# Kernel tuning notes

Measured on AMD Instinct MI355X. Metric: run time of the kernel, lower is better.

Reference implementation:

```python
import jax, jax.numpy as jnp
import numpy as np

DIM = 384
EPS = 1e-12  # F.normalize default eps


def setup_inputs() -> dict:
    key = jax.random.key(0)
    ks = jax.random.split(key, 6)
    b, c, h, w = 4, DIM, 64, 64
    x = jax.random.normal(ks[0], (b, c, h, w), dtype=jnp.float32)
    gamma = jnp.ones((c,), dtype=jnp.float32)  # WanRMS_norm gamma, init ones
    # 1x1 convs are per-pixel linear maps: [out_c, in_c] weight + bias
    w_qkv = jax.random.normal(ks[1], (3 * c, c), dtype=jnp.float32) * (1.0 / np.sqrt(c))
    b_qkv = jax.random.normal(ks[2], (3 * c,), dtype=jnp.float32) * 0.01
    w_proj = jax.random.normal(ks[3], (c, c), dtype=jnp.float32) * (1.0 / np.sqrt(c))
    b_proj = jax.random.normal(ks[4], (c,), dtype=jnp.float32) * 0.01
    return {"x": x, "gamma": gamma, "w_qkv": w_qkv, "b_qkv": b_qkv,
            "w_proj": w_proj, "b_proj": b_proj}


def reference(x, gamma, w_qkv, b_qkv, w_proj, b_proj):
    b, c, h, w = x.shape
    identity = x
    # WanRMS_norm: F.normalize over channel dim * sqrt(dim) * gamma
    l2 = jnp.sqrt(jnp.sum(x * x, axis=1, keepdims=True))
    xn = x / jnp.maximum(l2, EPS) * jnp.sqrt(jnp.float32(c)) * gamma[None, :, None, None]
    # 1x1 conv qkv: [b, 3c, h, w]
    qkv = jnp.einsum("bchw,oc->bohw", xn, w_qkv) + b_qkv[None, :, None, None]
    # flatten spatial -> tokens: [b, 3c, s] -> q/k/v each [b, s, c]
    s = h * w
    qkv = qkv.reshape(b, 3 * c, s).transpose(0, 2, 1)  # [b, s, 3c]
    q, k, v = jnp.split(qkv, 3, axis=-1)
    # single-head scaled dot-product attention (non-causal, as in Wan SDPA call)
    scores = jnp.einsum("bqc,bkc->bqk", q, k) / jnp.sqrt(jnp.float32(c))
    attn = jax.nn.softmax(scores, axis=-1)
    out = jnp.einsum("bqk,bkc->bqc", attn, v)  # [b, s, c]
    out = out.transpose(0, 2, 1).reshape(b, c, h, w)
    # 1x1 proj conv + residual
    out = jnp.einsum("bchw,oc->bohw", out, w_proj) + b_proj[None, :, None, None]
    return out + identity
```

## Files before the change

### kernel.cpp

```cpp
#include <hip/hip_runtime.h>
#include <cstdint>
#include <cstddef>

typedef __bf16 bf16;
typedef __bf16 bf16x8 __attribute__((ext_vector_type(8)));
typedef float  f32x4 __attribute__((ext_vector_type(4)));
typedef float  f32x16 __attribute__((ext_vector_type(16)));
typedef int    i32x4 __attribute__((ext_vector_type(4)));
typedef int    i32x8 __attribute__((ext_vector_type(8)));

#define MFMA16(a, b, c) __builtin_amdgcn_mfma_f32_16x16x32_bf16((a), (b), (c), 0, 0, 0)
#define MFMA_MX(a, b, c) \
    __builtin_amdgcn_mfma_scale_f32_32x32x64_f8f6f4((a), (b), (c), 0, 0, 0, 0x7F, 0, 0x7F)

__device__ __forceinline__ uint8_t to_fp8(float v) {
    return (uint8_t)(__builtin_amdgcn_cvt_pk_fp8_f32(v, v, 0, false) & 0xff);
}

__device__ __forceinline__ i32x8 ld32(const void* p) {
    i32x4 a = *(const i32x4*)p;
    i32x4 b = *(const i32x4*)((const char*)p + 16);
    i32x8 r;
    r[0] = a[0]; r[1] = a[1]; r[2] = a[2]; r[3] = a[3];
    r[4] = b[0]; r[5] = b[1]; r[6] = b[2]; r[7] = b[3];
    return r;
}

__device__ __forceinline__ void gload16(const void* g, void* l) {
    __builtin_amdgcn_global_load_lds(
        (const __attribute__((address_space(1))) unsigned int*)g,
        (__attribute__((address_space(3))) unsigned int*)l,
        16, 0, 0);
}

__global__ __launch_bounds__(256) void convert_w(
    const float* __restrict__ wqkv, const float* __restrict__ wproj,
    bf16* __restrict__ wq, bf16* __restrict__ wp)
{
    int t = blockIdx.x * 256 + threadIdx.x;
    if (t < 1152 * 384) wq[t] = (bf16)wqkv[t];
    else                wp[t - 1152 * 384] = (bf16)wproj[t - 1152 * 384];
}

__global__ __launch_bounds__(64) void norm_kernel(
    const float* __restrict__ x, const float* __restrict__ gamma,
    bf16* __restrict__ xn)
{
    __shared__ float sG[384];
    int tid = threadIdx.x;
    for (int i = tid; i < 384; i += 64) sG[i] = gamma[i];
    __syncthreads();
    int t = blockIdx.x * 64 + tid;
    int b = t >> 12, p = t & 4095;
    const float* xb = x + (size_t)(b * 384) * 4096 + p;
    float ss = 0.f;
    for (int c = 0; c < 384; ++c) { float v = xb[(size_t)c * 4096]; ss += v * v; }
    float scale = 19.595917942265423f / fmaxf(sqrtf(ss), 1e-12f);
    bf16* o = xn + (size_t)t * 384;
    for (int c0 = 0; c0 < 384; c0 += 8) {
        bf16x8 v8;
#pragma unroll
        for (int j = 0; j < 8; ++j)
            v8[j] = (bf16)(xb[(size_t)(c0 + j) * 4096] * scale * sG[c0 + j]);
        *(bf16x8*)(o + c0) = v8;
    }
}

__global__ __launch_bounds__(256) void gemm_bt(
    const bf16* __restrict__ A, const bf16* __restrict__ B,
    const float* __restrict__ bias_m, const float* __restrict__ bias_n,
    const float* __restrict__ resid, void* __restrict__ Cout,
    int mode, int ldc)
{
    __shared__ bf16 sA[128 * 72];
    __shared__ bf16 sB[128 * 72];
    const int tid = threadIdx.x;
    const int l = tid & 63, w = tid >> 6;
    const int lo = l & 15, hi = l >> 4;
    const int wm = w >> 1, wn = w & 1;
    const int m0 = blockIdx.y * 128, n0 = blockIdx.x * 128;

    f32x4 acc[4][4] = {};

    for (int kt = 0; kt < 6; ++kt) {
        __syncthreads();
        const int k0 = kt * 64;
#pragma unroll
        for (int i = 0; i < 5; ++i) {
            int ci = i * 256 + tid;
            if (ci < 1152) {
                int row = ci / 9, off = ci % 9;
                gload16(A + (size_t)(m0 + row) * 384 + k0 + off * 8, (char*)sA + ci * 16);
                gload16(B + (size_t)(n0 + row) * 384 + k0 + off * 8, (char*)sB + ci * 16);
            }
        }
        __syncthreads();
#pragma unroll
        for (int ks = 0; ks < 2; ++ks) {
            bf16x8 af[4], bfr[4];
#pragma unroll
            for (int t = 0; t < 4; ++t)
                af[t] = *(const bf16x8*)(sA + (wm * 64 + t * 16 + lo) * 72 + ks * 32 + hi * 8);
#pragma unroll
            for (int t = 0; t < 4; ++t)
                bfr[t] = *(const bf16x8*)(sB + (wn * 64 + t * 16 + lo) * 72 + ks * 32 + hi * 8);
#pragma unroll
            for (int rt = 0; rt < 4; ++rt)
#pragma unroll
                for (int ct = 0; ct < 4; ++ct)
                    acc[rt][ct] = MFMA16(af[rt], bfr[ct], acc[rt][ct]);
        }
    }

#pragma unroll
    for (int rt = 0; rt < 4; ++rt) {
#pragma unroll
        for (int ct = 0; ct < 4; ++ct) {
            int mb = m0 + wm * 64 + rt * 16 + hi * 4;
            int n  = n0 + wn * 64 + ct * 16 + lo;
            if (mode == 0) {
                uint8_t* C = (uint8_t*)Cout;
                float bn = bias_n[n];
#pragma unroll
                for (int r = 0; r < 4; ++r)
                    C[(size_t)(mb + r) * ldc + n] = to_fp8(acc[rt][ct][r] + bn);
            } else if (mode == 1) {
                uint8_t* C = (uint8_t*)Cout;
#pragma unroll
                for (int r = 0; r < 4; ++r)
                    C[(size_t)(mb + r) * ldc + n] = to_fp8(acc[rt][ct][r] + bias_m[mb + r]);
            } else {
                float* O = (float*)Cout;
                int bb = n >> 12, p = n & 4095;
#pragma unroll
                for (int r = 0; r < 4; ++r) {
                    int m = mb + r;
                    size_t idx = ((size_t)(bb * 384 + m)) * 4096 + p;
                    O[idx] = acc[rt][ct][r] + bias_m[m] + resid[idx];
                }
            }
        }
    }
}

__device__ __forceinline__ void stage_tiles64(
    const uint8_t* __restrict__ qk, const uint8_t* __restrict__ vt,
    int kv0, uint8_t* sK, uint8_t* sV, int tid)
{
    const uint8_t* kb = qk + (size_t)kv0 * 768 + 384;
#pragma unroll
    for (int i = 0; i < 7; ++i) {
        int ci = i * 256 + tid;
        if (ci < 1600) {
            int row = ci / 25, off = ci % 25;
            gload16(kb + (size_t)row * 768 + off * 16, sK + ci * 16);
        }
    }
    const uint8_t* vb = vt + kv0;
#pragma unroll
    for (int i = 0; i < 8; ++i) {
        int ci = i * 256 + tid;
        if (ci < 1920) {
            int row = ci / 5, off = ci % 5;
            gload16(vb + (size_t)row * 16384 + off * 16, sV + ci * 16);
        }
    }
}

__global__ __launch_bounds__(256, 2) void flash_kernel(
    const uint8_t* __restrict__ qk, const uint8_t* __restrict__ vt,
    bf16* __restrict__ op0, bf16* __restrict__ op1, float* __restrict__ ml)
{
    __shared__ char smem[56320];
    uint8_t* sK = (uint8_t*)smem;
    uint8_t* sV = (uint8_t*)smem + 25600;
    const int tid = threadIdx.x;
    const int l = tid & 63, w = tid >> 6;
    const int l31 = l & 31, hi2 = l >> 5;
    const int wq = w >> 1, wd = w & 1;
    const int qt = blockIdx.x, bh = blockIdx.y;
    const int b = bh >> 1, half = bh & 1;
    const int q0 = b * 4096 + qt * 64;
    const int kvbase = b * 4096 + half * 2048;
    const float SC = 0.07362217057594547f;

    i32x8 qf[6];
    {
        const uint8_t* qrow = qk + (size_t)(q0 + wq * 32 + l31) * 768 + hi2 * 32;
#pragma unroll
        for (int ksw = 0; ksw < 6; ++ksw)
            qf[ksw] = ld32(qrow + ksw * 64);
    }

    f32x16 o[6] = {};
    float m = -1e30f, lsum = 0.f;

    for (int kt = 0; kt < 32; ++kt) {
        stage_tiles64(qk, vt, kvbase + kt * 64, sK, sV, tid);
        __syncthreads();

        f32x16 s0 = {}, s1 = {};
#pragma unroll
        for (int ksw = 0; ksw < 6; ++ksw) {
            i32x8 ak0 = ld32(sK + (size_t)l31 * 400 + ksw * 64 + hi2 * 32);
            i32x8 ak1 = ld32(sK + (size_t)(32 + l31) * 400 + ksw * 64 + hi2 * 32);
            s0 = MFMA_MX(ak0, qf[ksw], s0);
            s1 = MFMA_MX(ak1, qf[ksw], s1);
        }

        float mx = s0[0];
#pragma unroll
        for (int r = 1; r < 16; ++r) mx = fmaxf(mx, s0[r]);
#pragma unroll
        for (int r = 0; r < 16; ++r) mx = fmaxf(mx, s1[r]);
        mx = fmaxf(mx, __shfl_xor(mx, 32));
        if (__any(mx > m)) {
            float mn = fmaxf(m, mx);
            float alpha = exp2f((m - mn) * SC);
            m = mn;
            lsum *= alpha;
#pragma unroll
            for (int dt = 0; dt < 6; ++dt)
#pragma unroll
                for (int r = 0; r < 16; ++r) o[dt][r] *= alpha;
        }
        float p0[16], p1[16];
        float rs = 0.f;
        float msc = m * SC;
#pragma unroll
        for (int r = 0; r < 16; ++r) { p0[r] = exp2f(fmaf(s0[r], SC, -msc)); rs += p0[r]; }
#pragma unroll
        for (int r = 0; r < 16; ++r) { p1[r] = exp2f(fmaf(s1[r], SC, -msc)); rs += p1[r]; }
        rs += __shfl_xor(rs, 32);
        lsum += rs;

        int pk0[4], pk1[4];
#pragma unroll
        for (int i = 0; i < 4; ++i) {
            int d = __builtin_amdgcn_cvt_pk_fp8_f32(p0[4 * i], p0[4 * i + 1], 0, false);
            pk0[i] = __builtin_amdgcn_cvt_pk_fp8_f32(p0[4 * i + 2], p0[4 * i + 3], d, true);
            d = __builtin_amdgcn_cvt_pk_fp8_f32(p1[4 * i], p1[4 * i + 1], 0, false);
            pk1[i] = __builtin_amdgcn_cvt_pk_fp8_f32(p1[4 * i + 2], p1[4 * i + 3], d, true);
        }
        i32x8 pf;
#pragma unroll
        for (int i = 0; i < 4; ++i) {
            int x0 = __shfl_xor(pk0[i], 32);
            int x1 = __shfl_xor(pk1[i], 32);
            int own = hi2 ? pk1[i] : pk0[i];
            int oth = hi2 ? x1 : x0;
            pf[2 * i]     = hi2 ? oth : own;
            pf[2 * i + 1] = hi2 ? own : oth;
        }

#pragma unroll
        for (int dt = 0; dt < 6; ++dt) {
            i32x8 av = ld32(sV + (size_t)(wd * 192 + dt * 32 + l31) * 80 + hi2 * 32);
            o[dt] = MFMA_MX(av, pf, o[dt]);
        }

        __syncthreads();
    }

    float* tr = (float*)(smem + w * 4608);
    bf16* dst = half ? op1 : op0;
#pragma unroll
    for (int dt = 0; dt < 6; ++dt) {
#pragma unroll
        for (int r = 0; r < 16; ++r) {
            int d32 = (r & 3) + 8 * (r >> 2) + 4 * hi2;
            tr[l31 * 36 + d32] = o[dt][r];
        }
        f32x4 v0 = *(f32x4*)(tr + l31 * 36 + hi2 * 16 + 0);
        f32x4 v1 = *(f32x4*)(tr + l31 * 36 + hi2 * 16 + 4);
        f32x4 v2 = *(f32x4*)(tr + l31 * 36 + hi2 * 16 + 8);
        f32x4 v3 = *(f32x4*)(tr + l31 * 36 + hi2 * 16 + 12);
        bf16x8 h0, h1;
#pragma unroll
        for (int j = 0; j < 4; ++j) {
            h0[j] = (bf16)v0[j]; h0[4 + j] = (bf16)v1[j];
            h1[j] = (bf16)v2[j]; h1[4 + j] = (bf16)v3[j];
        }
        size_t tok = (size_t)(q0 + wq * 32 + l31);
        bf16* drow = dst + tok * 384 + wd * 192 + dt * 32 + hi2 * 16;
        *(bf16x8*)(drow + 0) = h0;
        *(bf16x8*)(drow + 8) = h1;
        __syncthreads();
    }
    if (wd == 0 && hi2 == 0) {
        int tok = q0 + wq * 32 + l31;
        ml[(size_t)(half * 16384 + tok) * 2 + 0] = m * SC;
        ml[(size_t)(half * 16384 + tok) * 2 + 1] = lsum;
    }
}

__global__ __launch_bounds__(256) void merge_kernel(
    const bf16* __restrict__ p0, const bf16* __restrict__ p1,
    const float* __restrict__ ml, bf16* __restrict__ ob)
{
    int tok = blockIdx.x * 4 + (threadIdx.x >> 6);
    int l = threadIdx.x & 63;
    float m0 = ml[(size_t)tok * 2 + 0], l0 = ml[(size_t)tok * 2 + 1];
    float m1 = ml[(size_t)(16384 + tok) * 2 + 0], l1 = ml[(size_t)(16384 + tok) * 2 + 1];
    float mM = fmaxf(m0, m1);
    float a0 = exp2f(m0 - mM), a1 = exp2f(m1 - mM);
    float inv = 1.0f / (a0 * l0 + a1 * l1);
    float w0 = a0 * inv, w1 = a1 * inv;
    if (l < 48) {
        size_t off = (size_t)tok * 384 + l * 8;
        bf16x8 v0 = *(const bf16x8*)(p0 + off);
        bf16x8 v1 = *(const bf16x8*)(p1 + off);
        bf16x8 r;
#pragma unroll
        for (int j = 0; j < 8; ++j)
            r[j] = (bf16)((float)v0[j] * w0 + (float)v1[j] * w1);
        *(bf16x8*)(ob + off) = r;
    }
}

extern "C" void kernel_launch(void* const* d_in, const int* in_sizes, int n_in,
                              void* d_out, int out_size, void* d_ws, size_t ws_size,
                              hipStream_t stream) {
    const float* x      = (const float*)d_in[0];
    const float* gamma  = (const float*)d_in[1];
    const float* w_qkv  = (const float*)d_in[2];
    const float* b_qkv  = (const float*)d_in[3];
    const float* w_proj = (const float*)d_in[4];
    const float* b_proj = (const float*)d_in[5];
    float* out = (float*)d_out;

    char* ws = (char*)d_ws;
    bf16* xn  = (bf16*)ws;    ws += (size_t)16384 * 384 * 2;
    uint8_t* qkb = (uint8_t*)ws; ws += (size_t)16384 * 768;
    uint8_t* vtb = (uint8_t*)ws; ws += (size_t)384 * 16384;
    bf16* ob  = (bf16*)ws;    ws += (size_t)16384 * 384 * 2;
    bf16* wq  = (bf16*)ws;    ws += (size_t)1152 * 384 * 2;
    bf16* wp  = (bf16*)ws;    ws += (size_t)384 * 384 * 2;
    float* mlb = (float*)ws;  ws += (size_t)2 * 16384 * 2 * 4;

    convert_w<<<2304, 256, 0, stream>>>(w_qkv, w_proj, wq, wp);
    norm_kernel<<<256, 64, 0, stream>>>(x, gamma, xn);
    gemm_bt<<<dim3(6, 128), 256, 0, stream>>>(xn, wq, nullptr, b_qkv, nullptr, qkb, 0, 768);
    gemm_bt<<<dim3(128, 3), 256, 0, stream>>>(wq + (size_t)768 * 384, xn,
                                              b_qkv + 768, nullptr, nullptr, vtb, 1, 16384);
    flash_kernel<<<dim3(64, 8), 256, 0, stream>>>(qkb, vtb, xn, ob, mlb);
    merge_kernel<<<4096, 256, 0, stream>>>(xn, ob, mlb, ob);
    gemm_bt<<<dim3(128, 3), 256, 0, stream>>>(wp, ob, b_proj, nullptr, x, out, 2, 0);
}
```

Baseline: 287.4 us.

## Fuse weight conversion, norm, QKV GEMMs, merge; add lazy rescale and priorities

Folds the weight-conversion kernel into the norm kernel, which now splits the channel reduction across four waves for more parallelism. It merges the QK and V GEMMs into one launch, and fuses the split-KV merge into the projection GEMM's B-tile load. In the flash kernel it adds a lazy max-rescale threshold, raised wave priority around the MFMA sections, tree max reductions, split row-sum accumulators and a linearized grid. The aim is fewer launches, less intermediate traffic and more latency hiding. The risks are the fp8/exp2 overflow margin of the threshold and recomputing merge weights per tile row.

```diff
diff --git a/kernel.cpp b/kernel.cpp
--- a/kernel.cpp
+++ b/kernel.cpp
@@ -33,44 +33,142 @@
         16, 0, 0);
 }
 
-__global__ __launch_bounds__(256) void convert_w(
+__global__ __launch_bounds__(256) void norm_kernel(
+    const float* __restrict__ x, const float* __restrict__ gamma,
     const float* __restrict__ wqkv, const float* __restrict__ wproj,
-    bf16* __restrict__ wq, bf16* __restrict__ wp)
-{
-    int t = blockIdx.x * 256 + threadIdx.x;
-    if (t < 1152 * 384) wq[t] = (bf16)wqkv[t];
-    else                wp[t - 1152 * 384] = (bf16)wproj[t - 1152 * 384];
-}
-
-__global__ __launch_bounds__(64) void norm_kernel(
-    const float* __restrict__ x, const float* __restrict__ gamma,
-    bf16* __restrict__ xn)
-{
+    bf16* __restrict__ xn, bf16* __restrict__ wq, bf16* __restrict__ wp)
+{
+    const int tid = threadIdx.x;
+    const int blk = blockIdx.x;
+    if (blk >= 256) {
+        int t0 = (blk - 256) * 256 + tid;
+        for (int t = t0; t < 1152 * 384 + 384 * 384; t += 128 * 256) {
+            if (t < 1152 * 384) wq[t] = (bf16)wqkv[t];
+            else                wp[t - 1152 * 384] = (bf16)wproj[t - 1152 * 384];
+        }
+        return;
+    }
     __shared__ float sG[384];
-    int tid = threadIdx.x;
-    for (int i = tid; i < 384; i += 64) sG[i] = gamma[i];
+    __shared__ float sS[4][64];
+    __shared__ float sScale[64];
+    const int w = tid >> 6, l = tid & 63;
+    for (int i = tid; i < 384; i += 256) sG[i] = gamma[i];
+    const int b = blk >> 6, p0 = (blk & 63) << 6;
+    const float* xb = x + ((size_t)b * 384) * 4096 + p0 + l;
+    const float* xc = xb + (size_t)(96 * w) * 4096;
+    float s0 = 0.f, s1 = 0.f;
+#pragma unroll 8
+    for (int c = 0; c < 96; c += 2) {
+        float v0 = xc[(size_t)c * 4096];
+        float v1 = xc[(size_t)(c + 1) * 4096];
+        s0 += v0 * v0; s1 += v1 * v1;
+    }
+    sS[w][l] = s0 + s1;
     __syncthreads();
-    int t = blockIdx.x * 64 + tid;
-    int b = t >> 12, p = t & 4095;
-    const float* xb = x + (size_t)(b * 384) * 4096 + p;
-    float ss = 0.f;
-    for (int c = 0; c < 384; ++c) { float v = xb[(size_t)c * 4096]; ss += v * v; }
-    float scale = 19.595917942265423f / fmaxf(sqrtf(ss), 1e-12f);
-    bf16* o = xn + (size_t)t * 384;
-    for (int c0 = 0; c0 < 384; c0 += 8) {
+    if (w == 0) {
+        float t = (sS[0][l] + sS[1][l]) + (sS[2][l] + sS[3][l]);
+        sScale[l] = 19.595917942265423f / fmaxf(sqrtf(t), 1e-12f);
+    }
+    __syncthreads();
+    float sc = sScale[l];
+    int tok = (b << 12) + p0 + l;
+    bf16* o = xn + (size_t)tok * 384 + 96 * w;
+    for (int c0 = 0; c0 < 96; c0 += 8) {
         bf16x8 v8;
 #pragma unroll
         for (int j = 0; j < 8; ++j)
-            v8[j] = (bf16)(xb[(size_t)(c0 + j) * 4096] * scale * sG[c0 + j]);
+            v8[j] = (bf16)(xc[(size_t)(c0 + j) * 4096] * sc * sG[96 * w + c0 + j]);
         *(bf16x8*)(o + c0) = v8;
     }
 }
 
-__global__ __launch_bounds__(256) void gemm_bt(
+__device__ __forceinline__ void gemm_core_bt(
+    bf16* sA, bf16* sB,
     const bf16* __restrict__ A, const bf16* __restrict__ B,
     const float* __restrict__ bias_m, const float* __restrict__ bias_n,
-    const float* __restrict__ resid, void* __restrict__ Cout,
-    int mode, int ldc)
+    uint8_t* __restrict__ Cout, const int mode, const int ldc,
+    const int m0, const int n0)
+{
+    const int tid = threadIdx.x;
+    const int l = tid & 63, w = tid >> 6;
+    const int lo = l & 15, hi = l >> 4;
+    const int wm = w >> 1, wn = w & 1;
+
+    f32x4 acc[4][4] = {};
+
+    for (int kt = 0; kt < 6; ++kt) {
+        __syncthreads();
+        const int k0 = kt * 64;
+#pragma unroll
+        for (int i = 0; i < 5; ++i) {
+            int ci = i * 256 + tid;
+            if (ci < 1152) {
+                int row = ci / 9, off = ci % 9;
+                gload16(A + (size_t)(m0 + row) * 384 + k0 + off * 8, (char*)sA + ci * 16);
+                gload16(B + (size_t)(n0 + row) * 384 + k0 + off * 8, (char*)sB + ci * 16);
+            }
+        }
+        __syncthreads();
+#pragma unroll
+        for (int ks = 0; ks < 2; ++ks) {
+            bf16x8 af[4], bfr[4];
+#pragma unroll
+            for (int t = 0; t < 4; ++t)
+                af[t] = *(const bf16x8*)(sA + (wm * 64 + t * 16 + lo) * 72 + ks * 32 + hi * 8);
+#pragma unroll
+            for (int t = 0; t < 4; ++t)
+                bfr[t] = *(const bf16x8*)(sB + (wn * 64 + t * 16 + lo) * 72 + ks * 32 + hi * 8);
+#pragma unroll
+            for (int rt = 0; rt < 4; ++rt)
+#pragma unroll
+                for (int ct = 0; ct < 4; ++ct)
+                    acc[rt][ct] = MFMA16(af[rt], bfr[ct], acc[rt][ct]);
+        }
+    }
+
+#pragma unroll
+    for (int rt = 0; rt < 4; ++rt) {
+#pragma unroll
+        for (int ct = 0; ct < 4; ++ct) {
+            int mb = m0 + wm * 64 + rt * 16 + hi * 4;
+            int n  = n0 + wn * 64 + ct * 16 + lo;
+            if (mode == 0) {
+                float bn = bias_n[n];
+#pragma unroll
+                for (int r = 0; r < 4; ++r)
+                    Cout[(size_t)(mb + r) * ldc + n] = to_fp8(acc[rt][ct][r] + bn);
+            } else {
+#pragma unroll
+                for (int r = 0; r < 4; ++r)
+                    Cout[(size_t)(mb + r) * ldc + n] = to_fp8(acc[rt][ct][r] + bias_m[mb + r]);
+            }
+        }
+    }
+}
+
+__global__ __launch_bounds__(256) void gemm_qkv(
+    const bf16* __restrict__ xn, const bf16* __restrict__ wq,
+    const float* __restrict__ b_qkv, uint8_t* __restrict__ qkb,
+    uint8_t* __restrict__ vtb)
+{
+    __shared__ bf16 sA[128 * 72];
+    __shared__ bf16 sB[128 * 72];
+    const int id = blockIdx.x;
+    if (id < 768) {
+        gemm_core_bt(sA, sB, xn, wq, nullptr, b_qkv, qkb, 0, 768,
+                     (id / 6) * 128, (id % 6) * 128);
+    } else {
+        const int t = id - 768;
+        gemm_core_bt(sA, sB, wq + (size_t)768 * 384, xn, b_qkv + 768, nullptr,
+                     vtb, 1, 16384, (t >> 7) * 128, (t & 127) * 128);
+    }
+}
+
+__global__ __launch_bounds__(256) void gemm_proj(
+    const bf16* __restrict__ wp, const bf16* __restrict__ p0,
+    const bf16* __restrict__ p1, const float* __restrict__ ml,
+    const float* __restrict__ b_proj, const float* __restrict__ x,
+    float* __restrict__ out)
 {
     __shared__ bf16 sA[128 * 72];
     __shared__ bf16 sB[128 * 72];
@@ -90,8 +188,22 @@
             int ci = i * 256 + tid;
             if (ci < 1152) {
                 int row = ci / 9, off = ci % 9;
-                gload16(A + (size_t)(m0 + row) * 384 + k0 + off * 8, (char*)sA + ci * 16);
-                gload16(B + (size_t)(n0 + row) * 384 + k0 + off * 8, (char*)sB + ci * 16);
+                gload16(wp + (size_t)(m0 + row) * 384 + k0 + off * 8, (char*)sA + ci * 16);
+                int tok = n0 + row;
+                float2 ml0 = *(const float2*)(ml + (size_t)tok * 2);
+                float2 ml1 = *(const float2*)(ml + (size_t)(16384 + tok) * 2);
+                float mM = fmaxf(ml0.x, ml1.x);
+                float a0 = exp2f(ml0.x - mM), a1 = exp2f(ml1.x - mM);
+                float inv = 1.0f / (a0 * ml0.y + a1 * ml1.y);
+                float w0 = a0 * inv, w1 = a1 * inv;
+                size_t boff = (size_t)tok * 384 + k0 + off * 8;
+                bf16x8 v0 = *(const bf16x8*)(p0 + boff);
+                bf16x8 v1 = *(const bf16x8*)(p1 + boff);
+                bf16x8 r;
+#pragma unroll
+                for (int j = 0; j < 8; ++j)
+                    r[j] = (bf16)((float)v0[j] * w0 + (float)v1[j] * w1);
+                *(bf16x8*)((char*)sB + ci * 16) = r;
             }
         }
         __syncthreads();
@@ -118,26 +230,12 @@
         for (int ct = 0; ct < 4; ++ct) {
             int mb = m0 + wm * 64 + rt * 16 + hi * 4;
             int n  = n0 + wn * 64 + ct * 16 + lo;
-            if (mode == 0) {
-                uint8_t* C = (uint8_t*)Cout;
-                float bn = bias_n[n];
-#pragma unroll
-                for (int r = 0; r < 4; ++r)
-                    C[(size_t)(mb + r) * ldc + n] = to_fp8(acc[rt][ct][r] + bn);
-            } else if (mode == 1) {
-                uint8_t* C = (uint8_t*)Cout;
-#pragma unroll
-                for (int r = 0; r < 4; ++r)
-                    C[(size_t)(mb + r) * ldc + n] = to_fp8(acc[rt][ct][r] + bias_m[mb + r]);
-            } else {
-                float* O = (float*)Cout;
-                int bb = n >> 12, p = n & 4095;
-#pragma unroll
-                for (int r = 0; r < 4; ++r) {
-                    int m = mb + r;
-                    size_t idx = ((size_t)(bb * 384 + m)) * 4096 + p;
-                    O[idx] = acc[rt][ct][r] + bias_m[m] + resid[idx];
-                }
+            int bb = n >> 12, p = n & 4095;
+#pragma unroll
+            for (int r = 0; r < 4; ++r) {
+                int m = mb + r;
+                size_t idx = ((size_t)(bb * 384 + m)) * 4096 + p;
+                out[idx] = acc[rt][ct][r] + b_proj[m] + x[idx];
             }
         }
     }
@@ -178,11 +276,13 @@
     const int l = tid & 63, w = tid >> 6;
     const int l31 = l & 31, hi2 = l >> 5;
     const int wq = w >> 1, wd = w & 1;
-    const int qt = blockIdx.x, bh = blockIdx.y;
+    const int id = blockIdx.x;
+    const int qt = id >> 3, bh = id & 7;
     const int b = bh >> 1, half = bh & 1;
     const int q0 = b * 4096 + qt * 64;
     const int kvbase = b * 4096 + half * 2048;
     const float SC = 0.07362217057594547f;
+    const float THR = 108.664f;
 
     i32x8 qf[6];
     {
@@ -200,6 +300,7 @@
         __syncthreads();
 
         f32x16 s0 = {}, s1 = {};
+        __builtin_amdgcn_s_setprio(1);
 #pragma unroll
         for (int ksw = 0; ksw < 6; ++ksw) {
             i32x8 ak0 = ld32(sK + (size_t)l31 * 400 + ksw * 64 + hi2 * 32);
@@ -207,14 +308,20 @@
             s0 = MFMA_MX(ak0, qf[ksw], s0);
             s1 = MFMA_MX(ak1, qf[ksw], s1);
         }
-
-        float mx = s0[0];
-#pragma unroll
-        for (int r = 1; r < 16; ++r) mx = fmaxf(mx, s0[r]);
-#pragma unroll
-        for (int r = 0; r < 16; ++r) mx = fmaxf(mx, s1[r]);
+        __builtin_amdgcn_s_setprio(0);
+
+        float a0 = fmaxf(fmaxf(s0[0],  s0[1]),  fmaxf(s0[2],  s0[3]));
+        float a1 = fmaxf(fmaxf(s0[4],  s0[5]),  fmaxf(s0[6],  s0[7]));
+        float a2 = fmaxf(fmaxf(s0[8],  s0[9]),  fmaxf(s0[10], s0[11]));
+        float a3 = fmaxf(fmaxf(s0[12], s0[13]), fmaxf(s0[14], s0[15]));
+        float b0 = fmaxf(fmaxf(s1[0],  s1[1]),  fmaxf(s1[2],  s1[3]));
+        float b1 = fmaxf(fmaxf(s1[4],  s1[5]),  fmaxf(s1[6],  s1[7]));
+        float b2 = fmaxf(fmaxf(s1[8],  s1[9]),  fmaxf(s1[10], s1[11]));
+        float b3 = fmaxf(fmaxf(s1[12], s1[13]), fmaxf(s1[14], s1[15]));
+        float mx = fmaxf(fmaxf(fmaxf(a0, a1), fmaxf(a2, a3)),
+                         fmaxf(fmaxf(b0, b1), fmaxf(b2, b3)));
         mx = fmaxf(mx, __shfl_xor(mx, 32));
-        if (__any(mx > m)) {
+        if (__any(mx > m + THR)) {
             float mn = fmaxf(m, mx);
             float alpha = exp2f((m - mn) * SC);
             m = mn;
@@ -225,12 +332,23 @@
                 for (int r = 0; r < 16; ++r) o[dt][r] *= alpha;
         }
         float p0[16], p1[16];
-        float rs = 0.f;
         float msc = m * SC;
-#pragma unroll
-        for (int r = 0; r < 16; ++r) { p0[r] = exp2f(fmaf(s0[r], SC, -msc)); rs += p0[r]; }
-#pragma unroll
-        for (int r = 0; r < 16; ++r) { p1[r] = exp2f(fmaf(s1[r], SC, -msc)); rs += p1[r]; }
+        float rsa = 0.f, rsb = 0.f, rsc = 0.f, rsd = 0.f;
+#pragma unroll
+        for (int r = 0; r < 16; r += 4) {
+            p0[r]     = exp2f(fmaf(s0[r],     SC, -msc)); rsa += p0[r];
+            p0[r + 1] = exp2f(fmaf(s0[r + 1], SC, -msc)); rsb += p0[r + 1];
+            p0[r + 2] = exp2f(fmaf(s0[r + 2], SC, -msc)); rsc += p0[r + 2];
+            p0[r + 3] = exp2f(fmaf(s0[r + 3], SC, -msc)); rsd += p0[r + 3];
+        }
+#pragma unroll
+        for (int r = 0; r < 16; r += 4) {
+            p1[r]     = exp2f(fmaf(s1[r],     SC, -msc)); rsa += p1[r];
+            p1[r + 1] = exp2f(fmaf(s1[r + 1], SC, -msc)); rsb += p1[r + 1];
+            p1[r + 2] = exp2f(fmaf(s1[r + 2], SC, -msc)); rsc += p1[r + 2];
+            p1[r + 3] = exp2f(fmaf(s1[r + 3], SC, -msc)); rsd += p1[r + 3];
+        }
+        float rs = (rsa + rsb) + (rsc + rsd);
         rs += __shfl_xor(rs, 32);
         lsum += rs;
 
@@ -253,11 +371,13 @@
             pf[2 * i + 1] = hi2 ? own : oth;
         }
 
+        __builtin_amdgcn_s_setprio(1);
 #pragma unroll
         for (int dt = 0; dt < 6; ++dt) {
             i32x8 av = ld32(sV + (size_t)(wd * 192 + dt * 32 + l31) * 80 + hi2 * 32);
             o[dt] = MFMA_MX(av, pf, o[dt]);
         }
+        __builtin_amdgcn_s_setprio(0);
 
         __syncthreads();
     }
@@ -291,30 +411,6 @@
         int tok = q0 + wq * 32 + l31;
         ml[(size_t)(half * 16384 + tok) * 2 + 0] = m * SC;
         ml[(size_t)(half * 16384 + tok) * 2 + 1] = lsum;
-    }
-}
-
-__global__ __launch_bounds__(256) void merge_kernel(
-    const bf16* __restrict__ p0, const bf16* __restrict__ p1,
-    const float* __restrict__ ml, bf16* __restrict__ ob)
-{
-    int tok = blockIdx.x * 4 + (threadIdx.x >> 6);
-    int l = threadIdx.x & 63;
-    float m0 = ml[(size_t)tok * 2 + 0], l0 = ml[(size_t)tok * 2 + 1];
-    float m1 = ml[(size_t)(16384 + tok) * 2 + 0], l1 = ml[(size_t)(16384 + tok) * 2 + 1];
-    float mM = fmaxf(m0, m1);
-    float a0 = exp2f(m0 - mM), a1 = exp2f(m1 - mM);
-    float inv = 1.0f / (a0 * l0 + a1 * l1);
-    float w0 = a0 * inv, w1 = a1 * inv;
-    if (l < 48) {
-        size_t off = (size_t)tok * 384 + l * 8;
-        bf16x8 v0 = *(const bf16x8*)(p0 + off);
-        bf16x8 v1 = *(const bf16x8*)(p1 + off);
-        bf16x8 r;
-#pragma unroll
-        for (int j = 0; j < 8; ++j)
-            r[j] = (bf16)((float)v0[j] * w0 + (float)v1[j] * w1);
-        *(bf16x8*)(ob + off) = r;
     }
 }
 
@@ -334,16 +430,12 @@
     uint8_t* qkb = (uint8_t*)ws; ws += (size_t)16384 * 768;
     uint8_t* vtb = (uint8_t*)ws; ws += (size_t)384 * 16384;
     bf16* ob  = (bf16*)ws;    ws += (size_t)16384 * 384 * 2;
-    bf16* wq  = (bf16*)ws;    ws += (size_t)1152 * 384 * 2;
-    bf16* wp  = (bf16*)ws;    ws += (size_t)384 * 384 * 2;
+    bf16* wqb = (bf16*)ws;    ws += (size_t)1152 * 384 * 2;
+    bf16* wpb = (bf16*)ws;    ws += (size_t)384 * 384 * 2;
     float* mlb = (float*)ws;  ws += (size_t)2 * 16384 * 2 * 4;
 
-    convert_w<<<2304, 256, 0, stream>>>(w_qkv, w_proj, wq, wp);
-    norm_kernel<<<256, 64, 0, stream>>>(x, gamma, xn);
-    gemm_bt<<<dim3(6, 128), 256, 0, stream>>>(xn, wq, nullptr, b_qkv, nullptr, qkb, 0, 768);
-    gemm_bt<<<dim3(128, 3), 256, 0, stream>>>(wq + (size_t)768 * 384, xn,
-                                              b_qkv + 768, nullptr, nullptr, vtb, 1, 16384);
-    flash_kernel<<<dim3(64, 8), 256, 0, stream>>>(qkb, vtb, xn, ob, mlb);
-    merge_kernel<<<4096, 256, 0, stream>>>(xn, ob, mlb, ob);
-    gemm_bt<<<dim3(128, 3), 256, 0, stream>>>(wp, ob, b_proj, nullptr, x, out, 2, 0);
-}
+    norm_kernel<<<384, 256, 0, stream>>>(x, gamma, w_qkv, w_proj, xn, wqb, wpb);
+    gemm_qkv<<<1152, 256, 0, stream>>>(xn, wqb, b_qkv, qkb, vtb);
+    flash_kernel<<<512, 256, 0, stream>>>(qkb, vtb, xn, ob, mlb);
+    gemm_proj<<<dim3(128, 3), 256, 0, stream>>>(wpb, xn, ob, mlb, b_proj, x, out);
+}
```

After: 268.0 us. 6.7% less time.
